# Kernel tuning notes

Measured on AMD Instinct MI355X. Metric: run time of the kernel, lower is better.

## Reference

```python
import jax, jax.numpy as jnp
import numpy as np

L, B, S, D, H, DQ, DH = 6, 2, 1024, 1024, 16, 64, 4096  # layers, batch, seq, d_e, heads, d_q, d_h
EPS = 1e-5


def _ln(x, g, b):
    m = jnp.mean(x, axis=-1, keepdims=True)
    v = jnp.mean(jnp.square(x - m), axis=-1, keepdims=True)
    return (x - m) / jnp.sqrt(v + EPS) * g + b


def setup_inputs() -> dict:
    key = jax.random.key(0)
    ks = jax.random.split(key, 8)
    f = lambda k, shape: (jax.random.normal(k, shape, jnp.float32) * 0.02)
    return {
        "x": jax.random.normal(ks[0], (B, S, D), jnp.float32),
        "mask": jnp.zeros((B, S, S), dtype=bool),
        "Wq": f(ks[1], (L, D, H * DQ)), "bq": jnp.zeros((L, H * DQ), jnp.float32),
        "Wk": f(ks[2], (L, D, H * DQ)), "bk": jnp.zeros((L, H * DQ), jnp.float32),
        "Wv": f(ks[3], (L, D, H * DQ)), "bv": jnp.zeros((L, H * DQ), jnp.float32),
        "Wo": f(ks[4], (L, H * DQ, D)), "bo": jnp.zeros((L, D), jnp.float32),
        "ln1_g": jnp.ones((L, D), jnp.float32), "ln1_b": jnp.zeros((L, D), jnp.float32),
        "W1": f(ks[5], (L, D, DH)), "b1": jnp.zeros((L, DH), jnp.float32),
        "W2": f(ks[6], (L, DH, D)), "b2": jnp.zeros((L, D), jnp.float32),
        "ln2_g": jnp.ones((L, D), jnp.float32), "ln2_b": jnp.zeros((L, D), jnp.float32),
    }


def _encoder(x, mask, Wq, bq, Wk, bk, Wv, bv, Wo, bo, ln1_g, ln1_b, W1, b1, W2, b2, ln2_g, ln2_b):
    scale = 1.0 / np.sqrt(DQ).astype(np.float32)

    def step(h, p):
        wq, q_b, wk, k_b, wv, v_b, wo, o_b, g1, be1, w1, f_b1, w2, f_b2, g2, be2 = p
        q = (h @ wq + q_b).reshape(B, S, H, DQ)
        k = (h @ wk + k_b).reshape(B, S, H, DQ)
        v = (h @ wv + v_b).reshape(B, S, H, DQ)
        scores = jnp.einsum('bqhd,bkhd->bhqk', q, k) * scale  # [B,H,S,S]
        scores = jnp.where(mask[:, None, :, :], jnp.float32(-1e9), scores)
        attn = jax.nn.softmax(scores, axis=-1)
        ctx = jnp.einsum('bhqk,bkhd->bqhd', attn, v).reshape(B, S, H * DQ)
        h = _ln(h + ctx @ wo + o_b, g1, be1)
        ff = jax.nn.relu(h @ w1 + f_b1) @ w2 + f_b2  # 1x1 conv1d FFN == pointwise MLP
        h = _ln(h + ff, g2, be2)
        return h, None

    params = (Wq, bq, Wk, bk, Wv, bv, Wo, bo, ln1_g, ln1_b, W1, b1, W2, b2, ln2_g, ln2_b)
    out, _ = jax.lax.scan(step, x, params)
    return out


def reference(x, mask, Wq, bq, Wk, bk, Wv, bv, Wo, bo, ln1_g, ln1_b, W1, b1, W2, b2, ln2_g, ln2_b):
    return _encoder(x, mask, Wq, bq, Wk, bk, Wv, bv, Wo, bo, ln1_g, ln1_b, W1, b1, W2, b2, ln2_g, ln2_b)
```

## Files before the change

kernel.cpp:

```cpp
#include <hip/hip_runtime.h>


typedef unsigned short u16;
typedef __attribute__((ext_vector_type(8))) short bh8;
typedef __attribute__((ext_vector_type(4))) float f32x4;

#define PLANE (2048ull * 1024ull)

__device__ __forceinline__ u16 f2b(float f) {
    unsigned u = __float_as_uint(f);
    u += 0x7fffu + ((u >> 16) & 1u);
    return (u16)(u >> 16);
}
__device__ __forceinline__ void gl_lds16(const void* g, void* l) {
    __builtin_amdgcn_global_load_lds((const __attribute__((address_space(1))) void*)g,
                                     (__attribute__((address_space(3))) void*)l, 16, 0, 0);
}

#define MFMA(a, b, c) __builtin_amdgcn_mfma_f32_16x16x32_bf16((a), (b), (c), 0, 0, 0)

__device__ __forceinline__ void xcd_remap(int nx, int& bx, int& by) {
    int id = blockIdx.y * nx + blockIdx.x;
    int cpx = (nx * gridDim.y) >> 3;
    int sid = (id & 7) * cpx + (id >> 3);
    bx = sid & (nx - 1);
    by = sid / nx;
}

__global__ __launch_bounds__(256) void init_h(const float* __restrict__ x,
                                              u16* __restrict__ hbf, float* __restrict__ hf, int n4) {
    int i = blockIdx.x * 256 + threadIdx.x;
    if (i < n4) {
        float4 v = ((const float4*)x)[i];
        ((float4*)hf)[i] = v;
        u16 t[4] = { f2b(v.x), f2b(v.y), f2b(v.z), f2b(v.w) };
        ((ushort4*)hbf)[i] = *(const ushort4*)t;
    }
}

__device__ __forceinline__ void tp_tile_f2b(const float* __restrict__ in, u16* __restrict__ out,
                                            int R, int C, int ty, int tx) {
    const int r0 = ty * 64, c0 = tx * 64;
    __shared__ alignas(16) u16 tile[64][72];
    const int tid = threadIdx.x;
#pragma unroll
    for (int it = 0; it < 4; ++it) {
        int s = it * 256 + tid;
        int rr = s >> 4, c4 = (s & 15) * 4;
        const float* p = &in[(size_t)(r0 + rr) * C + c0 + c4];
        float d0 = p[0], d1 = p[1], d2 = p[2], d3 = p[3];
        u16 t[4] = { f2b(d0), f2b(d1), f2b(d2), f2b(d3) };
        *(ushort4*)&tile[rr][c4] = *(const ushort4*)t;
    }
    __syncthreads();
#pragma unroll
    for (int it = 0; it < 2; ++it) {
        int chunk = it * 256 + tid, cc = chunk >> 3, r8 = chunk & 7;
        u16 tmp[8];
#pragma unroll
        for (int j = 0; j < 8; ++j) tmp[j] = tile[r8 * 8 + j][cc];
        *(uint4*)&out[(size_t)(c0 + cc) * R + r0 + r8 * 8] = *(const uint4*)tmp;
    }
}

__global__ __launch_bounds__(256) void transpose_weights(
        const float* __restrict__ Wq, const float* __restrict__ Wk,
        const float* __restrict__ Wv, const float* __restrict__ Wo,
        const float* __restrict__ W1, const float* __restrict__ W2,
        u16* __restrict__ WT) {
    const int t = blockIdx.x;
    const int l = t / 3072, u = t - l * 3072;
    const size_t M1 = 1024ull * 1024ull;
    const float* wq = Wq + (size_t)l * M1;
    const float* wk = Wk + (size_t)l * M1;
    const float* wv = Wv + (size_t)l * M1;
    const float* wo = Wo + (size_t)l * M1;
    const float* w1 = W1 + (size_t)l * 4 * M1;
    const float* w2 = W2 + (size_t)l * 4 * M1;
    u16* base = WT + (size_t)l * 12 * M1;
    if (u < 1024) {
        int wsel = u >> 8, uu = u & 255;
        const float* src = wsel == 0 ? wq : wsel == 1 ? wk : wsel == 2 ? wv : wo;
        u16* dst = base + (size_t)wsel * M1;
        tp_tile_f2b(src, dst, 1024, 1024, uu >> 4, uu & 15);
    } else if (u < 2048) {
        int uu = u - 1024;
        tp_tile_f2b(w1, base + 4 * M1, 1024, 4096, uu >> 6, uu & 63);
    } else {
        int uu = u - 2048;
        tp_tile_f2b(w2, base + 8 * M1, 4096, 1024, uu >> 4, uu & 15);
    }
}

__device__ __forceinline__ void stage_ab(const u16* const ap[4], const u16* const bp[2],
                                         int koff, u16* As, u16* Bs, int tid) {
#pragma unroll
    for (int it = 0; it < 4; ++it) gl_lds16(ap[it] + koff, As + (it * 256 + tid) * 8);
#pragma unroll
    for (int it = 0; it < 2; ++it) gl_lds16(bp[it] + koff, Bs + (it * 256 + tid) * 8);
}

__device__ __forceinline__ void gemm_compute(const u16* As, const u16* Bs,
                                             int wave, int quad, int l16, f32x4 acc[2][4]) {
#pragma unroll
    for (int ks = 0; ks < 2; ++ks) {
        bh8 af[2], bf[4];
#pragma unroll
        for (int mi = 0; mi < 2; ++mi)
            af[mi] = *(const bh8*)&As[(wave * 32 + mi * 16 + l16) * 64 + ((ks * 4 + quad) ^ (l16 & 7)) * 8];
#pragma unroll
        for (int ni = 0; ni < 4; ++ni)
            bf[ni] = *(const bh8*)&Bs[(ni * 16 + l16) * 64 + ((ks * 4 + quad) ^ (l16 & 7)) * 8];
#pragma unroll
        for (int mi = 0; mi < 2; ++mi)
#pragma unroll
            for (int ni = 0; ni < 4; ++ni)
                acc[mi][ni] = MFMA(af[mi], bf[ni], acc[mi][ni]);
    }
}

__device__ __forceinline__ void gemm_loop64(const u16* __restrict__ A, const u16* __restrict__ BT,
                                            int K, int kb, int ke, int bm, int bn, f32x4 acc[2][4]) {
    __shared__ alignas(16) u16 As0[128 * 64];
    __shared__ alignas(16) u16 Bs0[64 * 64];
    __shared__ alignas(16) u16 As1[128 * 64];
    __shared__ alignas(16) u16 Bs1[64 * 64];
    const int tid = threadIdx.x;
    const int lane = tid & 63, wave = tid >> 6;
    const int quad = lane >> 4, l16 = lane & 15;

    const u16* ap[4];
    const u16* bp[2];
#pragma unroll
    for (int it = 0; it < 4; ++it) {
        int chunk = it * 256 + tid, row = chunk >> 3, sseg = (chunk & 7) ^ (row & 7);
        ap[it] = A + (size_t)(bm + row) * K + kb + sseg * 8;
    }
#pragma unroll
    for (int it = 0; it < 2; ++it) {
        int chunk = it * 256 + tid, row = chunk >> 3, sseg = (chunk & 7) ^ (row & 7);
        bp[it] = BT + (size_t)(bn + row) * K + kb + sseg * 8;
    }

    stage_ab(ap, bp, 0, As0, Bs0, tid);
    __syncthreads();
    for (int k0 = kb; k0 < ke; k0 += 128) {
        stage_ab(ap, bp, k0 + 64 - kb, As1, Bs1, tid);
        gemm_compute(As0, Bs0, wave, quad, l16, acc);
        __syncthreads();
        const bool more = (k0 + 128) < ke;
        if (more) stage_ab(ap, bp, k0 + 128 - kb, As0, Bs0, tid);
        gemm_compute(As1, Bs1, wave, quad, l16, acc);
        if (more) __syncthreads();
    }
}

__global__ __launch_bounds__(256) void qkv_gemm(const u16* __restrict__ A,
        const u16* __restrict__ BTq, const u16* __restrict__ BTk, const u16* __restrict__ BTv,
        const float* __restrict__ bq, const float* __restrict__ bk, const float* __restrict__ bv,
        u16* __restrict__ Oq, u16* __restrict__ Ok, u16* __restrict__ OvT) {
    int bx, by;
    xcd_remap(16, bx, by);
    const int z = blockIdx.z;
    const u16* BT = z == 0 ? BTq : (z == 1 ? BTk : BTv);
    const float* bias = z == 0 ? bq : (z == 1 ? bk : bv);
    const int bm = by * 128, bn = bx * 64;
    f32x4 acc[2][4] = {};
    gemm_loop64(A, BT, 1024, 0, 1024, bm, bn, acc);

    const int lane = threadIdx.x & 63, wave = threadIdx.x >> 6;
    const int quad = lane >> 4, l16 = lane & 15;
    const float scale = (z == 0) ? 0.125f : 1.0f;
#pragma unroll
    for (int mi = 0; mi < 2; ++mi) {
        int row0 = bm + wave * 32 + mi * 16 + quad * 4;
#pragma unroll
        for (int ni = 0; ni < 4; ++ni) {
            int col = bn + ni * 16 + l16;
            float bv_ = bias[col];
            if (z < 2) {
                u16* O = z == 0 ? Oq : Ok;
#pragma unroll
                for (int r = 0; r < 4; ++r)
                    O[(size_t)(row0 + r) * 1024 + col] = f2b((acc[mi][ni][r] + bv_) * scale);
            } else {
                int b = row0 >> 10, s0 = row0 & 1023;
                u16 tmp[4];
#pragma unroll
                for (int r = 0; r < 4; ++r) tmp[r] = f2b(acc[mi][ni][r] + bv_);
                *(ushort4*)&OvT[(size_t)(b * 1024 + col) * 1024 + s0] = *(const ushort4*)tmp;
            }
        }
    }
}

__global__ __launch_bounds__(256) void gemm_relu(const u16* __restrict__ A, const u16* __restrict__ BT,
        const float* __restrict__ bias, u16* __restrict__ Cb, int N, int K) {
    int bx, by;
    xcd_remap(64, bx, by);
    const int bm = by * 128, bn = bx * 64;
    f32x4 acc[2][4] = {};
    gemm_loop64(A, BT, K, 0, K, bm, bn, acc);
    const int lane = threadIdx.x & 63, wave = threadIdx.x >> 6;
    const int quad = lane >> 4, l16 = lane & 15;
#pragma unroll
    for (int mi = 0; mi < 2; ++mi) {
        int row0 = bm + wave * 32 + mi * 16 + quad * 4;
#pragma unroll
        for (int ni = 0; ni < 4; ++ni) {
            int col = bn + ni * 16 + l16;
            float bv = bias[col];
#pragma unroll
            for (int r = 0; r < 4; ++r)
                Cb[(size_t)(row0 + r) * N + col] = f2b(fmaxf(acc[mi][ni][r] + bv, 0.0f));
        }
    }
}

__global__ __launch_bounds__(256) void gemm_splitk(const u16* __restrict__ A, const u16* __restrict__ BT,
        float* __restrict__ P, int K, int slice) {
    int bx, by;
    xcd_remap(16, bx, by);
    const int bm = by * 128, bn = bx * 64, s = blockIdx.z;
    f32x4 acc[2][4] = {};
    gemm_loop64(A, BT, K, s * slice, (s + 1) * slice, bm, bn, acc);
    float* Pl = P + (size_t)s * PLANE;
    const int lane = threadIdx.x & 63, wave = threadIdx.x >> 6;
    const int quad = lane >> 4, l16 = lane & 15;
#pragma unroll
    for (int mi = 0; mi < 2; ++mi) {
        int row0 = bm + wave * 32 + mi * 16 + quad * 4;
#pragma unroll
        for (int ni = 0; ni < 4; ++ni) {
            int col = bn + ni * 16 + l16;
#pragma unroll
            for (int r = 0; r < 4; ++r)
                Pl[(size_t)(row0 + r) * 1024 + col] = acc[mi][ni][r];
        }
    }
}

__device__ __forceinline__ void attn_stageK(const u16* k, int b, int h, int kv0, u16* Ks) {
    const int tid = threadIdx.x;
#pragma unroll
    for (int i = 0; i < 2; ++i) {
        int chunk = i * 256 + tid, rr = chunk >> 3, seg = (chunk & 7) ^ (rr & 7);
        gl_lds16(k + (size_t)(b * 1024 + kv0 + rr) * 1024 + h * 64 + seg * 8, Ks + chunk * 8);
    }
}
__device__ __forceinline__ void attn_stageV(const u16* vT, int bh, int kv0, u16* VTs) {
    const int tid = threadIdx.x;
#pragma unroll
    for (int i = 0; i < 2; ++i) {
        int chunk = i * 256 + tid, rr = chunk >> 3, seg = (chunk & 7) ^ (rr & 7);
        gl_lds16(vT + (size_t)(bh * 64 + rr) * 1024 + kv0 + seg * 8, VTs + chunk * 8);
    }
}

__device__ __forceinline__ void attn_tile(const u16* Qs, const u16* Ksc, const u16* VTsc,
        u16* Ksn, u16* VTsn, u16* Psw, const u16* k, const u16* vT,
        const unsigned char* __restrict__ mask, int b, int h, int bh, int q0, int kv0, bool pre,
        int wave, int quad, int l16, float l[4], f32x4 o[4]) {
    if (pre) attn_stageK(k, b, h, kv0 + 64, Ksn);

    f32x4 st[4] = {};
#pragma unroll
    for (int ks = 0; ks < 2; ++ks) {
        bh8 a = *(const bh8*)&Qs[(wave * 16 + l16) * 64 + ((ks * 4 + quad) ^ (l16 & 7)) * 8];
#pragma unroll
        for (int ni = 0; ni < 4; ++ni) {
            bh8 bb = *(const bh8*)&Ksc[(ni * 16 + l16) * 64 + ((ks * 4 + quad) ^ (l16 & 7)) * 8];
            st[ni] = MFMA(a, bb, st[ni]);
        }
    }

#pragma unroll
    for (int r = 0; r < 4; ++r) {
        int qg = q0 + wave * 16 + quad * 4 + r;
        int prow = quad * 4 + r;
        float p[4], rs = 0.0f;
#pragma unroll
        for (int ni = 0; ni < 4; ++ni) {
            float sv = st[ni][r];
            int kg = kv0 + ni * 16 + l16;
            if (mask[(size_t)b * 1048576 + (size_t)qg * 1024 + kg]) sv = -1e9f;
            p[ni] = __expf(sv);
            rs += p[ni];
        }
#pragma unroll
        for (int off = 1; off < 16; off <<= 1) rs += __shfl_xor(rs, off, 64);
        l[r] += rs;
#pragma unroll
        for (int ni = 0; ni < 4; ++ni) {
            int cchunk = ((ni * 2) + (l16 >> 3)) ^ (prow & 7);
            Psw[prow * 64 + cchunk * 8 + (l16 & 7)] = f2b(p[ni]);
        }
    }
    __syncthreads();
    if (pre) attn_stageV(vT, bh, kv0 + 64, VTsn);

#pragma unroll
    for (int ks = 0; ks < 2; ++ks) {
        bh8 a = *(const bh8*)&Psw[l16 * 64 + ((ks * 4 + quad) ^ (l16 & 7)) * 8];
#pragma unroll
        for (int ni = 0; ni < 4; ++ni) {
            bh8 bb = *(const bh8*)&VTsc[(ni * 16 + l16) * 64 + ((ks * 4 + quad) ^ (l16 & 7)) * 8];
            o[ni] = MFMA(a, bb, o[ni]);
        }
    }
}

__global__ __launch_bounds__(256) void attn_kernel(const u16* __restrict__ q, const u16* __restrict__ k,
        const u16* __restrict__ vT, const unsigned char* __restrict__ mask, u16* __restrict__ ctx) {
    __shared__ alignas(16) u16 Qs[64 * 64];
    __shared__ alignas(16) u16 Ks0[64 * 64];
    __shared__ alignas(16) u16 Ks1[64 * 64];
    __shared__ alignas(16) u16 VTs0[64 * 64];
    __shared__ alignas(16) u16 VTs1[64 * 64];
    __shared__ alignas(16) u16 Ps[4][16 * 64];
    const int tid = threadIdx.x, lane = tid & 63, wave = tid >> 6;
    const int quad = lane >> 4, l16 = lane & 15;
    int bx, by;
    xcd_remap(16, bx, by);
    const int bh = by, b = bh >> 4, h = bh & 15;
    const int q0 = bx * 64;

#pragma unroll
    for (int i = 0; i < 2; ++i) {
        int chunk = i * 256 + tid, rr = chunk >> 3, seg = (chunk & 7) ^ (rr & 7);
        gl_lds16(q + (size_t)(b * 1024 + q0 + rr) * 1024 + h * 64 + seg * 8, Qs + chunk * 8);
    }
    attn_stageK(k, b, h, 0, Ks0);
    attn_stageV(vT, bh, 0, VTs0);
    __syncthreads();

    float l[4] = {0.0f, 0.0f, 0.0f, 0.0f};
    f32x4 o[4] = {};
    for (int kv0 = 0; kv0 < 1024; kv0 += 128) {
        attn_tile(Qs, Ks0, VTs0, Ks1, VTs1, Ps[wave], k, vT, mask, b, h, bh, q0,
                  kv0, true, wave, quad, l16, l, o);
        attn_tile(Qs, Ks1, VTs1, Ks0, VTs0, Ps[wave], k, vT, mask, b, h, bh, q0,
                  kv0 + 64, (kv0 + 128) < 1024, wave, quad, l16, l, o);
    }

#pragma unroll
    for (int r = 0; r < 4; ++r) {
        float inv = 1.0f / l[r];
#pragma unroll
        for (int ni = 0; ni < 4; ++ni) {
            size_t idx = (size_t)(b * 1024 + q0 + wave * 16 + quad * 4 + r) * 1024 + h * 64 + ni * 16 + l16;
            ctx[idx] = f2b(o[ni][r] * inv);
        }
    }
}

__global__ __launch_bounds__(256) void ln_reduce(const float* __restrict__ P, int np,
        const float* __restrict__ bias, const float* __restrict__ res,
        const float* __restrict__ g, const float* __restrict__ bb,
        u16* __restrict__ outb, float* __restrict__ outf) {
    const int row = blockIdx.x, tid = threadIdx.x;
    const int lane = tid & 63, wave = tid >> 6;
    const int c4 = tid * 4;
    const size_t base = (size_t)row * 1024 + c4;
    float4 t = *(const float4*)&res[base];
    float4 bi = *(const float4*)&bias[c4];
    t.x += bi.x; t.y += bi.y; t.z += bi.z; t.w += bi.w;
    for (int p = 0; p < np; ++p) {
        float4 q = *(const float4*)&P[(size_t)p * PLANE + base];
        t.x += q.x; t.y += q.y; t.z += q.z; t.w += q.w;
    }
    float s = t.x + t.y + t.z + t.w;
    float sq = t.x * t.x + t.y * t.y + t.z * t.z + t.w * t.w;
#pragma unroll
    for (int off = 32; off > 0; off >>= 1) { s += __shfl_down(s, off, 64); sq += __shfl_down(sq, off, 64); }
    __shared__ float ps[4], pq[4];
    if (lane == 0) { ps[wave] = s; pq[wave] = sq; }
    __syncthreads();
    s = ps[0] + ps[1] + ps[2] + ps[3];
    sq = pq[0] + pq[1] + pq[2] + pq[3];
    const float mean = s * (1.0f / 1024.0f);
    const float var = sq * (1.0f / 1024.0f) - mean * mean;
    const float rstd = rsqrtf(var + 1e-5f);
    float4 gg = *(const float4*)&g[c4];
    float4 bv = *(const float4*)&bb[c4];
    float y0 = (t.x - mean) * rstd * gg.x + bv.x;
    float y1 = (t.y - mean) * rstd * gg.y + bv.y;
    float y2 = (t.z - mean) * rstd * gg.z + bv.z;
    float y3 = (t.w - mean) * rstd * gg.w + bv.w;
    *(float4*)&outf[base] = make_float4(y0, y1, y2, y3);
    u16 ob[4] = { f2b(y0), f2b(y1), f2b(y2), f2b(y3) };
    *(ushort4*)&outb[base] = *(const ushort4*)ob;
}

extern "C" void kernel_launch(void* const* d_in, const int* in_sizes, int n_in,
                              void* d_out, int out_size, void* d_ws, size_t ws_size,
                              hipStream_t stream) {
    const float* x  = (const float*)d_in[0];
    const unsigned char* mask = (const unsigned char*)d_in[1];
    const float* Wq = (const float*)d_in[2];
    const float* bq = (const float*)d_in[3];
    const float* Wk = (const float*)d_in[4];
    const float* bk = (const float*)d_in[5];
    const float* Wv = (const float*)d_in[6];
    const float* bv = (const float*)d_in[7];
    const float* Wo = (const float*)d_in[8];
    const float* bo = (const float*)d_in[9];
    const float* g1 = (const float*)d_in[10];
    const float* be1= (const float*)d_in[11];
    const float* W1 = (const float*)d_in[12];
    const float* b1 = (const float*)d_in[13];
    const float* W2 = (const float*)d_in[14];
    const float* b2 = (const float*)d_in[15];
    const float* g2 = (const float*)d_in[16];
    const float* be2= (const float*)d_in[17];

    char* w = (char*)d_ws;
    const size_t MB = 1ull << 20;
    if (ws_size < 248 * MB) return;

    float* hf  = (float*)(w + 0 * MB);
    u16*   hbf = (u16*)  (w + 8 * MB);
    u16*   Qb  = (u16*)  (w + 12 * MB);
    u16*   Kb  = (u16*)  (w + 16 * MB);
    u16*   VTb = (u16*)  (w + 24 * MB);
    u16*   CTX = (u16*)  (w + 28 * MB);
    u16*   FF  = (u16*)  (w + 32 * MB);
    float* Pp  = (float*)(w + 72 * MB);
    u16*   WT6 = (u16*)  (w + 104 * MB);

    init_h<<<2048, 256, 0, stream>>>(x, hbf, hf, 512 * 1024);
    transpose_weights<<<18432, 256, 0, stream>>>(Wq, Wk, Wv, Wo, W1, W2, WT6);

    const size_t M1 = 1024ull * 1024ull;
    for (int l = 0; l < 6; ++l) {
        u16* base = WT6 + (size_t)l * 12 * M1;
        u16* WqT = base;
        u16* WkT = base + 1 * M1;
        u16* WvT = base + 2 * M1;
        u16* WoT = base + 3 * M1;
        u16* W1T = base + 4 * M1;
        u16* W2T = base + 8 * M1;

        qkv_gemm<<<dim3(16, 16, 3), 256, 0, stream>>>(hbf, WqT, WkT, WvT,
                bq + l * 1024, bk + l * 1024, bv + l * 1024, Qb, Kb, VTb);
        attn_kernel<<<dim3(16, 32), 256, 0, stream>>>(Qb, Kb, VTb, mask, CTX);
        gemm_splitk<<<dim3(16, 16, 2), 256, 0, stream>>>(CTX, WoT, Pp, 1024, 512);
        ln_reduce<<<2048, 256, 0, stream>>>(Pp, 2, bo + l * 1024, hf,
                g1 + l * 1024, be1 + l * 1024, hbf, hf);
        gemm_relu<<<dim3(64, 16), 256, 0, stream>>>(hbf, W1T, b1 + l * 4096, FF, 4096, 1024);
        gemm_splitk<<<dim3(16, 16, 4), 256, 0, stream>>>(FF, W2T, Pp, 4096, 1024);
        float* outf = (l == 5) ? (float*)d_out : hf;
        ln_reduce<<<2048, 256, 0, stream>>>(Pp, 4, b2 + l * 1024, hf,
                g2 + l * 1024, be2 + l * 1024, hbf, outf);
    }
}
```

Before: 1.266 ms.

## Widen FFN GEMM tiles to 128x128 and vectorize weight transpose loads

Templates the GEMM mainloop on the N-tile width and uses 128x128 block tiles for the FFN up-projection (relu) GEMM and the FFN down-projection split-K GEMM, halving block counts. This raises arithmetic intensity and reuse of the A tile per LDS stage, at the cost of more accumulator registers and LDS, which may lower occupancy. Separately, the weight transpose now loads float4 into a swizzled fp32 LDS tile and converts to bf16 on the way out.

Result: faster. 1.131 ms (-10.7%).

```diff
diff --git a/kernel.cpp b/kernel.cpp
--- a/kernel.cpp
+++ b/kernel.cpp
@@ -41,16 +41,15 @@
 __device__ __forceinline__ void tp_tile_f2b(const float* __restrict__ in, u16* __restrict__ out,
                                             int R, int C, int ty, int tx) {
     const int r0 = ty * 64, c0 = tx * 64;
-    __shared__ alignas(16) u16 tile[64][72];
+    __shared__ alignas(16) float tile[64][68];
     const int tid = threadIdx.x;
 #pragma unroll
     for (int it = 0; it < 4; ++it) {
         int s = it * 256 + tid;
         int rr = s >> 4, c4 = (s & 15) * 4;
-        const float* p = &in[(size_t)(r0 + rr) * C + c0 + c4];
-        float d0 = p[0], d1 = p[1], d2 = p[2], d3 = p[3];
-        u16 t[4] = { f2b(d0), f2b(d1), f2b(d2), f2b(d3) };
-        *(ushort4*)&tile[rr][c4] = *(const ushort4*)t;
+        float4 v = *(const float4*)&in[(size_t)(r0 + rr) * C + c0 + c4];
+        int gsw = ((c4 >> 2) ^ (rr >> 3)) << 2;
+        *(float4*)&tile[rr][gsw] = v;
     }
     __syncthreads();
 #pragma unroll
@@ -58,7 +57,11 @@
         int chunk = it * 256 + tid, cc = chunk >> 3, r8 = chunk & 7;
         u16 tmp[8];
 #pragma unroll
-        for (int j = 0; j < 8; ++j) tmp[j] = tile[r8 * 8 + j][cc];
+        for (int j = 0; j < 8; ++j) {
+            int r = r8 * 8 + j;
+            int col = ((((cc >> 2) ^ (r >> 3)) << 2) | (cc & 3));
+            tmp[j] = f2b(tile[r][col]);
+        }
         *(uint4*)&out[(size_t)(c0 + cc) * R + r0 + r8 * 8] = *(const uint4*)tmp;
     }
 }
@@ -92,65 +95,69 @@
     }
 }
 
-__device__ __forceinline__ void stage_ab(const u16* const ap[4], const u16* const bp[2],
+template<int NB>
+__device__ __forceinline__ void stage_ab(const u16* const ap[4], const u16* const bp[NB],
                                          int koff, u16* As, u16* Bs, int tid) {
 #pragma unroll
     for (int it = 0; it < 4; ++it) gl_lds16(ap[it] + koff, As + (it * 256 + tid) * 8);
 #pragma unroll
-    for (int it = 0; it < 2; ++it) gl_lds16(bp[it] + koff, Bs + (it * 256 + tid) * 8);
-}
-
+    for (int it = 0; it < NB; ++it) gl_lds16(bp[it] + koff, Bs + (it * 256 + tid) * 8);
+}
+
+template<int NI>
 __device__ __forceinline__ void gemm_compute(const u16* As, const u16* Bs,
-                                             int wave, int quad, int l16, f32x4 acc[2][4]) {
+                                             int wave, int quad, int l16, f32x4 acc[2][NI]) {
 #pragma unroll
     for (int ks = 0; ks < 2; ++ks) {
-        bh8 af[2], bf[4];
+        bh8 af[2], bf[NI];
 #pragma unroll
         for (int mi = 0; mi < 2; ++mi)
             af[mi] = *(const bh8*)&As[(wave * 32 + mi * 16 + l16) * 64 + ((ks * 4 + quad) ^ (l16 & 7)) * 8];
 #pragma unroll
-        for (int ni = 0; ni < 4; ++ni)
+        for (int ni = 0; ni < NI; ++ni)
             bf[ni] = *(const bh8*)&Bs[(ni * 16 + l16) * 64 + ((ks * 4 + quad) ^ (l16 & 7)) * 8];
 #pragma unroll
         for (int mi = 0; mi < 2; ++mi)
 #pragma unroll
-            for (int ni = 0; ni < 4; ++ni)
+            for (int ni = 0; ni < NI; ++ni)
                 acc[mi][ni] = MFMA(af[mi], bf[ni], acc[mi][ni]);
     }
 }
 
-__device__ __forceinline__ void gemm_loop64(const u16* __restrict__ A, const u16* __restrict__ BT,
-                                            int K, int kb, int ke, int bm, int bn, f32x4 acc[2][4]) {
+template<int NI>
+__device__ __forceinline__ void gemm_loopT(const u16* __restrict__ A, const u16* __restrict__ BT,
+                                           int K, int kb, int ke, int bm, int bn, f32x4 acc[2][NI]) {
+    constexpr int NB = NI / 2;
     __shared__ alignas(16) u16 As0[128 * 64];
-    __shared__ alignas(16) u16 Bs0[64 * 64];
+    __shared__ alignas(16) u16 Bs0[NI * 16 * 64];
     __shared__ alignas(16) u16 As1[128 * 64];
-    __shared__ alignas(16) u16 Bs1[64 * 64];
+    __shared__ alignas(16) u16 Bs1[NI * 16 * 64];
     const int tid = threadIdx.x;
     const int lane = tid & 63, wave = tid >> 6;
     const int quad = lane >> 4, l16 = lane & 15;
 
     const u16* ap[4];
-    const u16* bp[2];
+    const u16* bp[NB];
 #pragma unroll
     for (int it = 0; it < 4; ++it) {
         int chunk = it * 256 + tid, row = chunk >> 3, sseg = (chunk & 7) ^ (row & 7);
         ap[it] = A + (size_t)(bm + row) * K + kb + sseg * 8;
     }
 #pragma unroll
-    for (int it = 0; it < 2; ++it) {
+    for (int it = 0; it < NB; ++it) {
         int chunk = it * 256 + tid, row = chunk >> 3, sseg = (chunk & 7) ^ (row & 7);
         bp[it] = BT + (size_t)(bn + row) * K + kb + sseg * 8;
     }
 
-    stage_ab(ap, bp, 0, As0, Bs0, tid);
+    stage_ab<NB>(ap, bp, 0, As0, Bs0, tid);
     __syncthreads();
     for (int k0 = kb; k0 < ke; k0 += 128) {
-        stage_ab(ap, bp, k0 + 64 - kb, As1, Bs1, tid);
-        gemm_compute(As0, Bs0, wave, quad, l16, acc);
+        stage_ab<NB>(ap, bp, k0 + 64 - kb, As1, Bs1, tid);
+        gemm_compute<NI>(As0, Bs0, wave, quad, l16, acc);
         __syncthreads();
         const bool more = (k0 + 128) < ke;
-        if (more) stage_ab(ap, bp, k0 + 128 - kb, As0, Bs0, tid);
-        gemm_compute(As1, Bs1, wave, quad, l16, acc);
+        if (more) stage_ab<NB>(ap, bp, k0 + 128 - kb, As0, Bs0, tid);
+        gemm_compute<NI>(As1, Bs1, wave, quad, l16, acc);
         if (more) __syncthreads();
     }
 }
@@ -166,7 +173,7 @@
     const float* bias = z == 0 ? bq : (z == 1 ? bk : bv);
     const int bm = by * 128, bn = bx * 64;
     f32x4 acc[2][4] = {};
-    gemm_loop64(A, BT, 1024, 0, 1024, bm, bn, acc);
+    gemm_loopT<4>(A, BT, 1024, 0, 1024, bm, bn, acc);
 
     const int lane = threadIdx.x & 63, wave = threadIdx.x >> 6;
     const int quad = lane >> 4, l16 = lane & 15;
@@ -197,17 +204,17 @@
 __global__ __launch_bounds__(256) void gemm_relu(const u16* __restrict__ A, const u16* __restrict__ BT,
         const float* __restrict__ bias, u16* __restrict__ Cb, int N, int K) {
     int bx, by;
-    xcd_remap(64, bx, by);
-    const int bm = by * 128, bn = bx * 64;
-    f32x4 acc[2][4] = {};
-    gemm_loop64(A, BT, K, 0, K, bm, bn, acc);
+    xcd_remap(32, bx, by);
+    const int bm = by * 128, bn = bx * 128;
+    f32x4 acc[2][8] = {};
+    gemm_loopT<8>(A, BT, K, 0, K, bm, bn, acc);
     const int lane = threadIdx.x & 63, wave = threadIdx.x >> 6;
     const int quad = lane >> 4, l16 = lane & 15;
 #pragma unroll
     for (int mi = 0; mi < 2; ++mi) {
         int row0 = bm + wave * 32 + mi * 16 + quad * 4;
 #pragma unroll
-        for (int ni = 0; ni < 4; ++ni) {
+        for (int ni = 0; ni < 8; ++ni) {
             int col = bn + ni * 16 + l16;
             float bv = bias[col];
 #pragma unroll
@@ -217,13 +224,14 @@
     }
 }
 
+template<int NI>
 __global__ __launch_bounds__(256) void gemm_splitk(const u16* __restrict__ A, const u16* __restrict__ BT,
         float* __restrict__ P, int K, int slice) {
     int bx, by;
-    xcd_remap(16, bx, by);
-    const int bm = by * 128, bn = bx * 64, s = blockIdx.z;
-    f32x4 acc[2][4] = {};
-    gemm_loop64(A, BT, K, s * slice, (s + 1) * slice, bm, bn, acc);
+    xcd_remap(NI == 8 ? 8 : 16, bx, by);
+    const int bm = by * 128, bn = bx * (NI * 16), s = blockIdx.z;
+    f32x4 acc[2][NI] = {};
+    gemm_loopT<NI>(A, BT, K, s * slice, (s + 1) * slice, bm, bn, acc);
     float* Pl = P + (size_t)s * PLANE;
     const int lane = threadIdx.x & 63, wave = threadIdx.x >> 6;
     const int quad = lane >> 4, l16 = lane & 15;
@@ -231,7 +239,7 @@
     for (int mi = 0; mi < 2; ++mi) {
         int row0 = bm + wave * 32 + mi * 16 + quad * 4;
 #pragma unroll
-        for (int ni = 0; ni < 4; ++ni) {
+        for (int ni = 0; ni < NI; ++ni) {
             int col = bn + ni * 16 + l16;
 #pragma unroll
             for (int r = 0; r < 4; ++r)
@@ -444,11 +452,11 @@
         qkv_gemm<<<dim3(16, 16, 3), 256, 0, stream>>>(hbf, WqT, WkT, WvT,
                 bq + l * 1024, bk + l * 1024, bv + l * 1024, Qb, Kb, VTb);
         attn_kernel<<<dim3(16, 32), 256, 0, stream>>>(Qb, Kb, VTb, mask, CTX);
-        gemm_splitk<<<dim3(16, 16, 2), 256, 0, stream>>>(CTX, WoT, Pp, 1024, 512);
+        gemm_splitk<4><<<dim3(16, 16, 2), 256, 0, stream>>>(CTX, WoT, Pp, 1024, 512);
         ln_reduce<<<2048, 256, 0, stream>>>(Pp, 2, bo + l * 1024, hf,
                 g1 + l * 1024, be1 + l * 1024, hbf, hf);
-        gemm_relu<<<dim3(64, 16), 256, 0, stream>>>(hbf, W1T, b1 + l * 4096, FF, 4096, 1024);
-        gemm_splitk<<<dim3(16, 16, 4), 256, 0, stream>>>(FF, W2T, Pp, 4096, 1024);
+        gemm_relu<<<dim3(32, 16), 256, 0, stream>>>(hbf, W1T, b1 + l * 4096, FF, 4096, 1024);
+        gemm_splitk<8><<<dim3(8, 16, 4), 256, 0, stream>>>(FF, W2T, Pp, 4096, 1024);
         float* outf = (l == 5) ? (float*)d_out : hf;
         ln_reduce<<<2048, 256, 0, stream>>>(Pp, 4, b2 + l * 1024, hf,
                 g2 + l * 1024, be2 + l * 1024, hbf, outf);
```
